# Kernel tuning notes

Measured on AMD Instinct MI355X. Metric: run time of the kernel, lower is better.

Reference implementation:

```python
import jax, jax.numpy as jnp
import numpy as np

N = 100000
E = 1600000
IN_DIM, H1, H2, H3 = 128, 128, 64, 32


def gcn_conv(x, edge_index, W, b, n):
    # PyG GCNConv (default): add self-loops, symmetric norm D^-1/2 (A+I) D^-1/2,
    # out[dst] = sum_{src->dst} norm * (x @ W)[src] + b
    src, dst = edge_index[0], edge_index[1]
    loops = jnp.arange(n)
    src = jnp.concatenate([src, loops])
    dst = jnp.concatenate([dst, loops])
    deg = jax.ops.segment_sum(jnp.ones((src.shape[0],), dtype=x.dtype), dst, num_segments=n)
    dinv = jnp.where(deg > 0, jax.lax.rsqrt(deg), jnp.zeros((), dtype=x.dtype))
    norm = dinv[src] * dinv[dst]  # [E+N]
    h = x @ W                      # [N, out_dim] dense transform first (out_dim <= in_dim)
    msg = h[src] * norm[:, None]   # [E+N, out_dim] gather + scale
    out = jax.ops.segment_sum(msg, dst, num_segments=n)
    return out + b


def setup_inputs() -> dict:
    key = jax.random.key(0)
    ks = jax.random.split(key, 10)
    def glorot(k, shape):
        lim = np.sqrt(6.0 / (shape[0] + shape[1]))
        return jax.random.uniform(k, shape, jnp.float32, -lim, lim)
    return {
        "x": jax.random.normal(ks[0], (N, IN_DIM), jnp.float32),
        "edge_index": jax.random.randint(ks[1], (2, E), 0, N, jnp.int64),
        "W1": glorot(ks[2], (IN_DIM, H1)), "b1": jnp.zeros((H1,), jnp.float32),
        "W2": glorot(ks[3], (H1, H2)),     "b2": jnp.zeros((H2,), jnp.float32),
        "W3": glorot(ks[4], (H2, H3)),     "b3": jnp.zeros((H3,), jnp.float32),
        "Wl": glorot(ks[5], (H3, 1)),      "bl": jnp.zeros((1,), jnp.float32),
    }


def reference(x, edge_index, W1, b1, W2, b2, W3, b3, Wl, bl):
    n = x.shape[0]
    h = jax.nn.relu(gcn_conv(x, edge_index, W1, b1, n))   # dropout p=0.5 is identity in eval
    h = jax.nn.relu(gcn_conv(h, edge_index, W2, b2, n))
    h = jax.nn.relu(gcn_conv(h, edge_index, W3, b3, n))
    return jax.nn.sigmoid(h @ Wl + bl)                    # [N, 1]
```

## Files before the change

### kernel.cpp

```cpp
#include <hip/hip_runtime.h>
#include <hip/hip_fp16.h>
#include <math.h>


#define BSHIFT 8
#define BNODES (1 << BSHIFT)
#define SRCBITS 17
#define MAXB 512
#define CHUNK 16384

union H8 { float4 f4; __half2 h2[4]; };

typedef _Float16 half8 __attribute__((ext_vector_type(8)));
typedef float floatx4 __attribute__((ext_vector_type(4)));

__global__ __launch_bounds__(256) void k_hist2(const int* __restrict__ dst, int E,
                                               int* __restrict__ cnt_mat, int B) {
    __shared__ int h[MAXB];
    int tid = threadIdx.x, c = blockIdx.x;
    h[tid] = 0; h[tid + 256] = 0;
    __syncthreads();
    int base = c * CHUNK, end = min(base + CHUNK, E);
    for (int i = base + tid; i < end; i += 256)
        atomicAdd(&h[dst[i] >> BSHIFT], 1);
    __syncthreads();
    for (int b = tid; b < B; b += 256) cnt_mat[c * B + b] = h[b];
}

__global__ __launch_bounds__(256) void k_colscan(const int* __restrict__ cnt_mat,
                                                 int* __restrict__ rel_mat,
                                                 int* __restrict__ total,
                                                 int B, int nchunks) {
    __shared__ int s[256];
    int b = blockIdx.x, tid = threadIdx.x;
    int v = (tid < nchunks) ? cnt_mat[tid * B + b] : 0;
    s[tid] = v;
    __syncthreads();
    for (int off = 1; off < 256; off <<= 1) {
        int t = (tid >= off) ? s[tid - off] : 0;
        __syncthreads();
        s[tid] += t;
        __syncthreads();
    }
    if (tid < nchunks) rel_mat[tid * B + b] = s[tid] - v;
    if (tid == 255) total[b] = s[255];
}

__global__ __launch_bounds__(512) void k_bscan(const int* __restrict__ total,
                                               int* __restrict__ bucketbase,
                                               int* __restrict__ row_ptr,
                                               int B, int n, int E) {
    __shared__ int s[MAXB];
    int tid = threadIdx.x;
    int v = (tid < B) ? total[tid] : 0;
    s[tid] = v;
    __syncthreads();
    for (int off = 1; off < MAXB; off <<= 1) {
        int t = (tid >= off) ? s[tid - off] : 0;
        __syncthreads();
        s[tid] += t;
        __syncthreads();
    }
    if (tid < B) bucketbase[tid] = s[tid] - v;
    if (tid == 0) { bucketbase[B] = E; row_ptr[n] = E; }
}

__global__ __launch_bounds__(256) void k_bucket2(const int* __restrict__ src,
                                                 const int* __restrict__ dst, int E,
                                                 const int* __restrict__ bucketbase,
                                                 const int* __restrict__ rel_mat,
                                                 unsigned int* __restrict__ edgebuf,
                                                 int B) {
    __shared__ int cur[MAXB];
    int c = blockIdx.x, tid = threadIdx.x;
    int base = c * CHUNK, end = min(base + CHUNK, E);
    for (int b = tid; b < B; b += 256) cur[b] = bucketbase[b] + rel_mat[c * B + b];
    __syncthreads();
    for (int i = base + tid; i < end; i += 256) {
        int d = dst[i];
        int b = d >> BSHIFT;
        unsigned int pk = ((unsigned int)(d & (BNODES - 1)) << SRCBITS) | (unsigned int)src[i];
        int pos = atomicAdd(&cur[b], 1);
        edgebuf[pos] = pk;
    }
}

__global__ __launch_bounds__(256) void k_build(const unsigned int* __restrict__ edgebuf,
                                               const int* __restrict__ bucketbase,
                                               int* __restrict__ row_ptr,
                                               float* __restrict__ dinv,
                                               int* __restrict__ col, int n) {
    __shared__ int cnt[BNODES];
    __shared__ int s[BNODES];
    int b = blockIdx.x;
    int tid = threadIdx.x;
    int node0 = b << BSHIFT;
    int ebase = bucketbase[b], eend = bucketbase[b + 1];
    cnt[tid] = 0;
    __syncthreads();
    for (int i = ebase + tid; i < eend; i += 256)
        atomicAdd(&cnt[edgebuf[i] >> SRCBITS], 1);
    __syncthreads();
    int c = cnt[tid];
    s[tid] = c;
    __syncthreads();
    for (int off = 1; off < 256; off <<= 1) {
        int t = (tid >= off) ? s[tid - off] : 0;
        __syncthreads();
        s[tid] += t;
        __syncthreads();
    }
    int p = ebase + s[tid] - c;
    int node = node0 + tid;
    if (node < n) { row_ptr[node] = p; dinv[node] = rsqrtf((float)(c + 1)); }
    cnt[tid] = p;
    __syncthreads();
    for (int i = ebase + tid; i < eend; i += 256) {
        unsigned int pk = edgebuf[i];
        int pos = atomicAdd(&cnt[pk >> SRCBITS], 1);
        col[pos] = (int)(pk & ((1u << SRCBITS) - 1));
    }
}

__global__ void k_packW3(const float* __restrict__ W1, const float* __restrict__ W2,
                         const float* __restrict__ W3, _Float16* __restrict__ P1,
                         _Float16* __restrict__ P2, _Float16* __restrict__ P3) {
    int e = blockIdx.x * 256 + threadIdx.x;
    const float* W; _Float16* P; int OUT, idx;
    if (e < 16384)      { W = W1; P = P1; OUT = 128; idx = e; }
    else if (e < 24576) { W = W2; P = P2; OUT = 64;  idx = e - 16384; }
    else if (e < 26624) { W = W3; P = P3; OUT = 32;  idx = e - 24576; }
    else return;
    int j = idx & 7;
    int lane = (idx >> 3) & 63;
    int rest = idx >> 9;
    int NT = OUT >> 4;
    int t = rest % NT;
    int ss = rest / NT;
    int k = ss * 32 + (lane >> 4) * 8 + j;
    int nn = t * 16 + (lane & 15);
    P[idx] = (_Float16)W[k * OUT + nn];
}

template <int IN, int OUT>
__global__ __launch_bounds__(256) void k_matmul_mfma(const float* __restrict__ x,
                                                     const _Float16* __restrict__ Wpk,
                                                     const float* __restrict__ dinv,
                                                     __half* __restrict__ out, int n) {
    constexpr int S = IN / 32;
    constexpr int NT = OUT / 16;
    constexpr int LDH = IN + 8;
    __shared__ _Float16 xs[64 * LDH];

    int tid = threadIdx.x;
    int rowbase = blockIdx.x * 64;

    constexpr int TOT = 64 * IN / 8;
    const float4* x4 = (const float4*)x;
    for (int i = tid; i < TOT; i += 256) {
        int r = i / (IN / 8), kg = i % (IN / 8);
        int row = rowbase + r;
        float4 a = make_float4(0.f, 0.f, 0.f, 0.f), b = a;
        if (row < n) {
            a = x4[(size_t)row * (IN / 4) + kg * 2 + 0];
            b = x4[(size_t)row * (IN / 4) + kg * 2 + 1];
        }
        H8 u;
        u.h2[0] = __float22half2_rn(make_float2(a.x, a.y));
        u.h2[1] = __float22half2_rn(make_float2(a.z, a.w));
        u.h2[2] = __float22half2_rn(make_float2(b.x, b.y));
        u.h2[3] = __float22half2_rn(make_float2(b.z, b.w));
        *(float4*)&xs[r * LDH + kg * 8] = u.f4;
    }
    __syncthreads();

    int lane = tid & 63;
    int wave = tid >> 6;
    int m = lane & 15, quad = lane >> 4;

    floatx4 acc[NT];
#pragma unroll
    for (int t = 0; t < NT; ++t) acc[t] = (floatx4){0.f, 0.f, 0.f, 0.f};

    const half8* Wf = (const half8*)Wpk;
#pragma unroll
    for (int s = 0; s < S; ++s) {
        half8 a = *(const half8*)&xs[(wave * 16 + m) * LDH + s * 32 + quad * 8];
#pragma unroll
        for (int t = 0; t < NT; ++t) {
            half8 b = Wf[(s * NT + t) * 64 + lane];
            acc[t] = __builtin_amdgcn_mfma_f32_16x16x32_f16(a, b, acc[t], 0, 0, 0);
        }
    }

    int rbase = rowbase + wave * 16 + quad * 4;
#pragma unroll
    for (int r = 0; r < 4; ++r) {
        int row = rbase + r;
        if (row < n) {
            float dsc = dinv[row];
#pragma unroll
            for (int t = 0; t < NT; ++t)
                out[(size_t)row * OUT + t * 16 + m] = __float2half(acc[t][r] * dsc);
        }
    }
}

template <int F, int OUT>
__global__ __launch_bounds__(256) void k_agg_mm(const __half* __restrict__ hs,
                                                const float* __restrict__ dinv,
                                                const float* __restrict__ bias,
                                                const int* __restrict__ row_ptr,
                                                const int* __restrict__ col,
                                                const _Float16* __restrict__ Wpk,
                                                __half* __restrict__ out, int n) {
    constexpr int S = F / 32;
    constexpr int NT = OUT / 16;
    constexpr int LDH = F + 8;
    constexpr int LPN = F / 8;
    __shared__ _Float16 zs[64 * LDH];

    int tid = threadIdx.x;
    int rowbase = blockIdx.x * 64;
    const float4* h4 = (const float4*)hs;

    for (int task = tid; task < 64 * LPN; task += 256) {
        int nl = task / LPN;
        int fg = task % LPN;
        int node = rowbase + nl;
        H8 o;
        if (node < n) {
            float acc[8];
            H8 u;
            u.f4 = h4[(size_t)node * LPN + fg];
#pragma unroll
            for (int q = 0; q < 4; ++q) {
                float2 f = __half22float2(u.h2[q]);
                acc[2 * q + 0] = f.x;
                acc[2 * q + 1] = f.y;
            }
            int beg = row_ptr[node], end = row_ptr[node + 1];
            int j = beg;
            for (; j + 3 < end; j += 4) {
                int s0 = col[j], s1 = col[j + 1], s2 = col[j + 2], s3 = col[j + 3];
                H8 u0, u1, u2, u3;
                u0.f4 = h4[(size_t)s0 * LPN + fg];
                u1.f4 = h4[(size_t)s1 * LPN + fg];
                u2.f4 = h4[(size_t)s2 * LPN + fg];
                u3.f4 = h4[(size_t)s3 * LPN + fg];
#pragma unroll
                for (int q = 0; q < 4; ++q) {
                    float2 f0 = __half22float2(u0.h2[q]);
                    float2 f1 = __half22float2(u1.h2[q]);
                    float2 f2 = __half22float2(u2.h2[q]);
                    float2 f3 = __half22float2(u3.h2[q]);
                    acc[2 * q + 0] += (f0.x + f1.x) + (f2.x + f3.x);
                    acc[2 * q + 1] += (f0.y + f1.y) + (f2.y + f3.y);
                }
            }
            for (; j < end; ++j) {
                H8 u2;
                u2.f4 = h4[(size_t)col[j] * LPN + fg];
#pragma unroll
                for (int q = 0; q < 4; ++q) {
                    float2 f = __half22float2(u2.h2[q]);
                    acc[2 * q + 0] += f.x;
                    acc[2 * q + 1] += f.y;
                }
            }
            float dsc = dinv[node];
#pragma unroll
            for (int q = 0; q < 4; ++q) {
                float v0 = fmaxf(fmaf(acc[2 * q + 0], dsc, bias[fg * 8 + 2 * q + 0]), 0.f);
                float v1 = fmaxf(fmaf(acc[2 * q + 1], dsc, bias[fg * 8 + 2 * q + 1]), 0.f);
                o.h2[q] = __floats2half2_rn(v0, v1);
            }
        } else {
            o.f4 = make_float4(0.f, 0.f, 0.f, 0.f);
        }
        *(float4*)&zs[nl * LDH + fg * 8] = o.f4;
    }
    __syncthreads();

    int lane = tid & 63;
    int wave = tid >> 6;
    int m = lane & 15, quad = lane >> 4;

    floatx4 acc[NT];
#pragma unroll
    for (int t = 0; t < NT; ++t) acc[t] = (floatx4){0.f, 0.f, 0.f, 0.f};

    const half8* Wf = (const half8*)Wpk;
#pragma unroll
    for (int s = 0; s < S; ++s) {
        half8 a = *(const half8*)&zs[(wave * 16 + m) * LDH + s * 32 + quad * 8];
#pragma unroll
        for (int t = 0; t < NT; ++t) {
            half8 b = Wf[(s * NT + t) * 64 + lane];
            acc[t] = __builtin_amdgcn_mfma_f32_16x16x32_f16(a, b, acc[t], 0, 0, 0);
        }
    }

    int rbase = rowbase + wave * 16 + quad * 4;
#pragma unroll
    for (int r = 0; r < 4; ++r) {
        int row = rbase + r;
        if (row < n) {
            float dsc = dinv[row];
#pragma unroll
            for (int t = 0; t < NT; ++t)
                out[(size_t)row * OUT + t * 16 + m] = __float2half(acc[t][r] * dsc);
        }
    }
}

__global__ __launch_bounds__(256) void k_agg_final(const __half* __restrict__ hs,
                                                   const float* __restrict__ dinv,
                                                   const float* __restrict__ bias,
                                                   const int* __restrict__ row_ptr,
                                                   const int* __restrict__ col,
                                                   const float* __restrict__ Wl,
                                                   const float* __restrict__ bl,
                                                   float* __restrict__ out, int n) {
    constexpr int LPN = 4;
    int t = blockIdx.x * 256 + threadIdx.x;
    int node = t / LPN;
    int fg = t % LPN;
    if (node >= n) return;

    const float4* h4 = (const float4*)hs;
    float acc[8];
    {
        H8 u;
        u.f4 = h4[(size_t)node * LPN + fg];
#pragma unroll
        for (int q = 0; q < 4; ++q) {
            float2 f = __half22float2(u.h2[q]);
            acc[2 * q + 0] = f.x;
            acc[2 * q + 1] = f.y;
        }
    }
    int beg = row_ptr[node], end = row_ptr[node + 1];
    int j = beg;
    for (; j + 3 < end; j += 4) {
        int s0 = col[j], s1 = col[j + 1], s2 = col[j + 2], s3 = col[j + 3];
        H8 u0, u1, u2, u3;
        u0.f4 = h4[(size_t)s0 * LPN + fg];
        u1.f4 = h4[(size_t)s1 * LPN + fg];
        u2.f4 = h4[(size_t)s2 * LPN + fg];
        u3.f4 = h4[(size_t)s3 * LPN + fg];
#pragma unroll
        for (int q = 0; q < 4; ++q) {
            float2 f0 = __half22float2(u0.h2[q]);
            float2 f1 = __half22float2(u1.h2[q]);
            float2 f2 = __half22float2(u2.h2[q]);
            float2 f3 = __half22float2(u3.h2[q]);
            acc[2 * q + 0] += (f0.x + f1.x) + (f2.x + f3.x);
            acc[2 * q + 1] += (f0.y + f1.y) + (f2.y + f3.y);
        }
    }
    for (; j < end; ++j) {
        H8 u;
        u.f4 = h4[(size_t)col[j] * LPN + fg];
#pragma unroll
        for (int q = 0; q < 4; ++q) {
            float2 f = __half22float2(u.h2[q]);
            acc[2 * q + 0] += f.x;
            acc[2 * q + 1] += f.y;
        }
    }
    float dsc = dinv[node];
    float partial = 0.f;
#pragma unroll
    for (int k = 0; k < 8; ++k) {
        float v = fmaxf(fmaf(acc[k], dsc, bias[fg * 8 + k]), 0.f);
        partial = fmaf(v, Wl[fg * 8 + k], partial);
    }
    partial += __shfl_xor(partial, 1);
    partial += __shfl_xor(partial, 2);
    if (fg == 0) out[node] = 1.f / (1.f + expf(-(partial + bl[0])));
}

extern "C" void kernel_launch(void* const* d_in, const int* in_sizes, int n_in,
                              void* d_out, int out_size, void* d_ws, size_t ws_size,
                              hipStream_t stream) {
    const float* x  = (const float*)d_in[0];
    const int*   ei = (const int*)d_in[1];
    const float* W1 = (const float*)d_in[2];
    const float* b1 = (const float*)d_in[3];
    const float* W2 = (const float*)d_in[4];
    const float* b2 = (const float*)d_in[5];
    const float* W3 = (const float*)d_in[6];
    const float* b3 = (const float*)d_in[7];
    const float* Wl = (const float*)d_in[8];
    const float* bl = (const float*)d_in[9];

    const int N = in_sizes[0] / 128;
    const int E = in_sizes[1] / 2;
    const int* src = ei;
    const int* dst = ei + E;
    const int B = (N + BNODES - 1) >> BSHIFT;
    const int NC = (E + CHUNK - 1) / CHUNK;

    char* ws = (char*)d_ws;
    size_t off = 0;
    auto take = [&](size_t bytes) -> char* {
        char* p = ws + off;
        off += (bytes + 255) & ~(size_t)255;
        return p;
    };
    int*          cnt_mat    = (int*)take((size_t)NC * B * 4);
    int*          rel_mat    = (int*)take((size_t)NC * B * 4);
    int*          total      = (int*)take(MAXB * 4);
    int*          bucketbase = (int*)take((MAXB + 1) * 4);
    unsigned int* edgebuf    = (unsigned int*)take((size_t)E * 4);
    int*          row_ptr    = (int*)take((size_t)(N + 1) * 4);
    float*        dinv       = (float*)take((size_t)N * 4);
    int*          col        = (int*)take((size_t)E * 4);
    __half*       bufA       = (__half*)take((size_t)N * 128 * 2);
    __half*       bufB       = (__half*)take((size_t)N * 128 * 2);
    _Float16*     Wpk1       = (_Float16*)take(128 * 128 * 2);
    _Float16*     Wpk2       = (_Float16*)take(128 * 64 * 2);
    _Float16*     Wpk3       = (_Float16*)take(64 * 32 * 2);
    (void)ws_size;

    int gM = (N + 63) / 64;

    k_hist2<<<NC, 256, 0, stream>>>(dst, E, cnt_mat, B);
    k_colscan<<<B, 256, 0, stream>>>(cnt_mat, rel_mat, total, B, NC);
    k_bscan<<<1, MAXB, 0, stream>>>(total, bucketbase, row_ptr, B, N, E);
    k_bucket2<<<NC, 256, 0, stream>>>(src, dst, E, bucketbase, rel_mat, edgebuf, B);
    k_build<<<B, 256, 0, stream>>>(edgebuf, bucketbase, row_ptr, dinv, col, N);

    k_packW3<<<(26624 + 255) / 256, 256, 0, stream>>>(W1, W2, W3, Wpk1, Wpk2, Wpk3);

    k_matmul_mfma<128, 128><<<gM, 256, 0, stream>>>(x, Wpk1, dinv, bufA, N);

    k_agg_mm<128, 64><<<gM, 256, 0, stream>>>(bufA, dinv, b1, row_ptr, col, Wpk2, bufB, N);

    k_agg_mm<64, 32><<<gM, 256, 0, stream>>>(bufB, dinv, b2, row_ptr, col, Wpk3, bufA, N);

    k_agg_final<<<((size_t)N * 4 + 255) / 256, 256, 0, stream>>>(
        bufA, dinv, b3, row_ptr, col, Wl, bl, (float*)d_out, N);
}
```

Baseline: 297.9 us.

## Split fused aggregate-matmul into feature-sliced gather and separate MFMA matmul

Replaces the fused aggregate+matmul kernels with separate steps. The matmul writes its output in 16-feature slices, one contiguous slice array per feature group. A new aggregation kernel then gathers one slice at a time across node blocks, so each gathered working set is a narrow 32-byte row per node, which is meant to improve cache hit rates on random neighbor gathers. The cost is extra kernel launches and an extra full write and read of the aggregated features between the gather and the matmul.

```diff
diff --git a/kernel.cpp b/kernel.cpp
--- a/kernel.cpp
+++ b/kernel.cpp
@@ -142,11 +142,12 @@
     P[idx] = (_Float16)W[k * OUT + nn];
 }
 
-template <int IN, int OUT>
-__global__ __launch_bounds__(256) void k_matmul_mfma(const float* __restrict__ x,
+template <int IN, int OUT, bool XHALF, bool SLICED>
+__global__ __launch_bounds__(256) void k_matmul_mfma(const void* __restrict__ xv,
                                                      const _Float16* __restrict__ Wpk,
                                                      const float* __restrict__ dinv,
-                                                     __half* __restrict__ out, int n) {
+                                                     __half* __restrict__ out, int n,
+                                                     int n16) {
     constexpr int S = IN / 32;
     constexpr int NT = OUT / 16;
     constexpr int LDH = IN + 8;
@@ -156,21 +157,27 @@
     int rowbase = blockIdx.x * 64;
 
     constexpr int TOT = 64 * IN / 8;
-    const float4* x4 = (const float4*)x;
+    const float4* x4 = (const float4*)xv;
     for (int i = tid; i < TOT; i += 256) {
         int r = i / (IN / 8), kg = i % (IN / 8);
         int row = rowbase + r;
-        float4 a = make_float4(0.f, 0.f, 0.f, 0.f), b = a;
-        if (row < n) {
-            a = x4[(size_t)row * (IN / 4) + kg * 2 + 0];
-            b = x4[(size_t)row * (IN / 4) + kg * 2 + 1];
-        }
-        H8 u;
-        u.h2[0] = __float22half2_rn(make_float2(a.x, a.y));
-        u.h2[1] = __float22half2_rn(make_float2(a.z, a.w));
-        u.h2[2] = __float22half2_rn(make_float2(b.x, b.y));
-        u.h2[3] = __float22half2_rn(make_float2(b.z, b.w));
-        *(float4*)&xs[r * LDH + kg * 8] = u.f4;
+        if (XHALF) {
+            float4 v = make_float4(0.f, 0.f, 0.f, 0.f);
+            if (row < n) v = x4[(size_t)row * (IN / 8) + kg];
+            *(float4*)&xs[r * LDH + kg * 8] = v;
+        } else {
+            float4 a = make_float4(0.f, 0.f, 0.f, 0.f), b = a;
+            if (row < n) {
+                a = x4[(size_t)row * (IN / 4) + kg * 2 + 0];
+                b = x4[(size_t)row * (IN / 4) + kg * 2 + 1];
+            }
+            H8 u;
+            u.h2[0] = __float22half2_rn(make_float2(a.x, a.y));
+            u.h2[1] = __float22half2_rn(make_float2(a.z, a.w));
+            u.h2[2] = __float22half2_rn(make_float2(b.x, b.y));
+            u.h2[3] = __float22half2_rn(make_float2(b.z, b.w));
+            *(float4*)&xs[r * LDH + kg * 8] = u.f4;
+        }
     }
     __syncthreads();
 
@@ -200,118 +207,81 @@
         if (row < n) {
             float dsc = dinv[row];
 #pragma unroll
-            for (int t = 0; t < NT; ++t)
-                out[(size_t)row * OUT + t * 16 + m] = __float2half(acc[t][r] * dsc);
-        }
-    }
-}
-
-template <int F, int OUT>
-__global__ __launch_bounds__(256) void k_agg_mm(const __half* __restrict__ hs,
-                                                const float* __restrict__ dinv,
-                                                const float* __restrict__ bias,
-                                                const int* __restrict__ row_ptr,
-                                                const int* __restrict__ col,
-                                                const _Float16* __restrict__ Wpk,
-                                                __half* __restrict__ out, int n) {
-    constexpr int S = F / 32;
-    constexpr int NT = OUT / 16;
-    constexpr int LDH = F + 8;
-    constexpr int LPN = F / 8;
-    __shared__ _Float16 zs[64 * LDH];
-
+            for (int t = 0; t < NT; ++t) {
+                __half v = __float2half(acc[t][r] * dsc);
+                if (SLICED) out[((size_t)t * n16 + row) * 16 + m] = v;
+                else        out[(size_t)row * OUT + t * 16 + m] = v;
+            }
+        }
+    }
+}
+
+template <int F, int NSL>
+__global__ __launch_bounds__(256) void k_agg_slice(const __half* __restrict__ hs_s,
+                                                   const float* __restrict__ dinv,
+                                                   const float* __restrict__ bias,
+                                                   const int* __restrict__ row_ptr,
+                                                   const int* __restrict__ col,
+                                                   __half* __restrict__ z, int n,
+                                                   int n16) {
+    int fg = blockIdx.x % NSL;
+    int nr = blockIdx.x / NSL;
     int tid = threadIdx.x;
-    int rowbase = blockIdx.x * 64;
-    const float4* h4 = (const float4*)hs;
-
-    for (int task = tid; task < 64 * LPN; task += 256) {
-        int nl = task / LPN;
-        int fg = task % LPN;
-        int node = rowbase + nl;
-        H8 o;
-        if (node < n) {
-            float acc[8];
-            H8 u;
-            u.f4 = h4[(size_t)node * LPN + fg];
-#pragma unroll
-            for (int q = 0; q < 4; ++q) {
-                float2 f = __half22float2(u.h2[q]);
-                acc[2 * q + 0] = f.x;
-                acc[2 * q + 1] = f.y;
-            }
-            int beg = row_ptr[node], end = row_ptr[node + 1];
-            int j = beg;
-            for (; j + 3 < end; j += 4) {
-                int s0 = col[j], s1 = col[j + 1], s2 = col[j + 2], s3 = col[j + 3];
-                H8 u0, u1, u2, u3;
-                u0.f4 = h4[(size_t)s0 * LPN + fg];
-                u1.f4 = h4[(size_t)s1 * LPN + fg];
-                u2.f4 = h4[(size_t)s2 * LPN + fg];
-                u3.f4 = h4[(size_t)s3 * LPN + fg];
-#pragma unroll
-                for (int q = 0; q < 4; ++q) {
-                    float2 f0 = __half22float2(u0.h2[q]);
-                    float2 f1 = __half22float2(u1.h2[q]);
-                    float2 f2 = __half22float2(u2.h2[q]);
-                    float2 f3 = __half22float2(u3.h2[q]);
-                    acc[2 * q + 0] += (f0.x + f1.x) + (f2.x + f3.x);
-                    acc[2 * q + 1] += (f0.y + f1.y) + (f2.y + f3.y);
-                }
-            }
-            for (; j < end; ++j) {
-                H8 u2;
-                u2.f4 = h4[(size_t)col[j] * LPN + fg];
-#pragma unroll
-                for (int q = 0; q < 4; ++q) {
-                    float2 f = __half22float2(u2.h2[q]);
-                    acc[2 * q + 0] += f.x;
-                    acc[2 * q + 1] += f.y;
-                }
-            }
-            float dsc = dinv[node];
-#pragma unroll
-            for (int q = 0; q < 4; ++q) {
-                float v0 = fmaxf(fmaf(acc[2 * q + 0], dsc, bias[fg * 8 + 2 * q + 0]), 0.f);
-                float v1 = fmaxf(fmaf(acc[2 * q + 1], dsc, bias[fg * 8 + 2 * q + 1]), 0.f);
-                o.h2[q] = __floats2half2_rn(v0, v1);
-            }
-        } else {
-            o.f4 = make_float4(0.f, 0.f, 0.f, 0.f);
-        }
-        *(float4*)&zs[nl * LDH + fg * 8] = o.f4;
-    }
-    __syncthreads();
-
-    int lane = tid & 63;
-    int wave = tid >> 6;
-    int m = lane & 15, quad = lane >> 4;
-
-    floatx4 acc[NT];
-#pragma unroll
-    for (int t = 0; t < NT; ++t) acc[t] = (floatx4){0.f, 0.f, 0.f, 0.f};
-
-    const half8* Wf = (const half8*)Wpk;
-#pragma unroll
-    for (int s = 0; s < S; ++s) {
-        half8 a = *(const half8*)&zs[(wave * 16 + m) * LDH + s * 32 + quad * 8];
-#pragma unroll
-        for (int t = 0; t < NT; ++t) {
-            half8 b = Wf[(s * NT + t) * 64 + lane];
-            acc[t] = __builtin_amdgcn_mfma_f32_16x16x32_f16(a, b, acc[t], 0, 0, 0);
-        }
-    }
-
-    int rbase = rowbase + wave * 16 + quad * 4;
-#pragma unroll
-    for (int r = 0; r < 4; ++r) {
-        int row = rbase + r;
-        if (row < n) {
-            float dsc = dinv[row];
-#pragma unroll
-            for (int t = 0; t < NT; ++t)
-                out[(size_t)row * OUT + t * 16 + m] = __float2half(acc[t][r] * dsc);
-        }
-    }
+    int node = nr * 128 + (tid >> 1);
+    int sub = tid & 1;
+    if (node >= n) return;
+
+    const float4* h4 = (const float4*)(hs_s + (size_t)fg * n16 * 16);
+    float acc[8];
+    {
+        H8 u;
+        u.f4 = h4[(size_t)node * 2 + sub];
+#pragma unroll
+        for (int q = 0; q < 4; ++q) {
+            float2 f = __half22float2(u.h2[q]);
+            acc[2 * q + 0] = f.x;
+            acc[2 * q + 1] = f.y;
+        }
+    }
+    int beg = row_ptr[node], end = row_ptr[node + 1];
+    int j = beg;
+    for (; j + 3 < end; j += 4) {
+        int s0 = col[j], s1 = col[j + 1], s2 = col[j + 2], s3 = col[j + 3];
+        H8 u0, u1, u2, u3;
+        u0.f4 = h4[(size_t)s0 * 2 + sub];
+        u1.f4 = h4[(size_t)s1 * 2 + sub];
+        u2.f4 = h4[(size_t)s2 * 2 + sub];
+        u3.f4 = h4[(size_t)s3 * 2 + sub];
+#pragma unroll
+        for (int q = 0; q < 4; ++q) {
+            float2 f0 = __half22float2(u0.h2[q]);
+            float2 f1 = __half22float2(u1.h2[q]);
+            float2 f2 = __half22float2(u2.h2[q]);
+            float2 f3 = __half22float2(u3.h2[q]);
+            acc[2 * q + 0] += (f0.x + f1.x) + (f2.x + f3.x);
+            acc[2 * q + 1] += (f0.y + f1.y) + (f2.y + f3.y);
+        }
+    }
+    for (; j < end; ++j) {
+        H8 u;
+        u.f4 = h4[(size_t)col[j] * 2 + sub];
+#pragma unroll
+        for (int q = 0; q < 4; ++q) {
+            float2 f = __half22float2(u.h2[q]);
+            acc[2 * q + 0] += f.x;
+            acc[2 * q + 1] += f.y;
+        }
+    }
+    float dsc = dinv[node];
+    int fbase = fg * 16 + sub * 8;
+    H8 o;
+#pragma unroll
+    for (int q = 0; q < 4; ++q) {
+        float v0 = fmaxf(fmaf(acc[2 * q + 0], dsc, bias[fbase + 2 * q + 0]), 0.f);
+        float v1 = fmaxf(fmaf(acc[2 * q + 1], dsc, bias[fbase + 2 * q + 1]), 0.f);
+        o.h2[q] = __floats2half2_rn(v0, v1);
+    }
+    *(float4*)(z + (size_t)node * F + fbase) = o.f4;
 }
 
 __global__ __launch_bounds__(256) void k_agg_final(const __half* __restrict__ hs,
@@ -401,6 +371,7 @@
     const int* dst = ei + E;
     const int B = (N + BNODES - 1) >> BSHIFT;
     const int NC = (E + CHUNK - 1) / CHUNK;
+    const int N16 = (N + 127) & ~127;
 
     char* ws = (char*)d_ws;
     size_t off = 0;
@@ -417,8 +388,8 @@
     int*          row_ptr    = (int*)take((size_t)(N + 1) * 4);
     float*        dinv       = (float*)take((size_t)N * 4);
     int*          col        = (int*)take((size_t)E * 4);
-    __half*       bufA       = (__half*)take((size_t)N * 128 * 2);
-    __half*       bufB       = (__half*)take((size_t)N * 128 * 2);
+    __half*       bufA       = (__half*)take((size_t)N16 * 128 * 2);
+    __half*       bufB       = (__half*)take((size_t)N16 * 128 * 2);
     _Float16*     Wpk1       = (_Float16*)take(128 * 128 * 2);
     _Float16*     Wpk2       = (_Float16*)take(128 * 64 * 2);
     _Float16*     Wpk3       = (_Float16*)take(64 * 32 * 2);
@@ -434,12 +405,15 @@
 
     k_packW3<<<(26624 + 255) / 256, 256, 0, stream>>>(W1, W2, W3, Wpk1, Wpk2, Wpk3);
 
-    k_matmul_mfma<128, 128><<<gM, 256, 0, stream>>>(x, Wpk1, dinv, bufA, N);
-
-    k_agg_mm<128, 64><<<gM, 256, 0, stream>>>(bufA, dinv, b1, row_ptr, col, Wpk2, bufB, N);
-
-    k_agg_mm<64, 32><<<gM, 256, 0, stream>>>(bufB, dinv, b2, row_ptr, col, Wpk3, bufA, N);
-
+    k_matmul_mfma<128, 128, false, true><<<gM, 256, 0, stream>>>(x, Wpk1, dinv, bufA, N, N16);
+    k_agg_slice<128, 8><<<((N + 127) / 128) * 8, 256, 0, stream>>>(
+        bufA, dinv, b1, row_ptr, col, bufB, N, N16);
+
+    k_matmul_mfma<128, 64, true, true><<<gM, 256, 0, stream>>>(bufB, Wpk2, dinv, bufA, N, N16);
+    k_agg_slice<64, 4><<<((N + 127) / 128) * 4, 256, 0, stream>>>(
+        bufA, dinv, b2, row_ptr, col, bufB, N, N16);
+
+    k_matmul_mfma<64, 32, true, false><<<gM, 256, 0, stream>>>(bufB, Wpk3, dinv, bufA, N, N16);
     k_agg_final<<<((size_t)N * 4 + 255) / 256, 256, 0, stream>>>(
         bufA, dinv, b3, row_ptr, col, Wl, bl, (float*)d_out, N);
 }
```

Measured after the change: 376.1 us. 1.26x slower.

## Fuse CSR preprocessing scans into partition and first matmul into CSR build

Applied to the files above, without the earlier changes.

Merges weight packing into the histogram launch. Replaces the column and bucket scans with per-block redundant prefix computation inside the partition kernel. Fuses the first dense transform into the per-bucket CSR build kernel, reusing locally computed degree normalisation. Halves the chunk size. This removes several kernel launches and intermediate buffers, at the cost of redundant scan work per block and fewer, heavier blocks for the first matmul.

```diff
diff --git a/kernel.cpp b/kernel.cpp
--- a/kernel.cpp
+++ b/kernel.cpp
@@ -7,17 +7,44 @@
 #define BNODES (1 << BSHIFT)
 #define SRCBITS 17
 #define MAXB 512
-#define CHUNK 16384
+#define CHUNK 8192
+#define PACKB 104
 
 union H8 { float4 f4; __half2 h2[4]; };
 
 typedef _Float16 half8 __attribute__((ext_vector_type(8)));
 typedef float floatx4 __attribute__((ext_vector_type(4)));
 
-__global__ __launch_bounds__(256) void k_hist2(const int* __restrict__ dst, int E,
-                                               int* __restrict__ cnt_mat, int B) {
+__global__ __launch_bounds__(256) void k_hist_pack(const int* __restrict__ dst, int E,
+                                                   int* __restrict__ cnt_mat, int B,
+                                                   int NC,
+                                                   const float* __restrict__ W1,
+                                                   const float* __restrict__ W2,
+                                                   const float* __restrict__ W3,
+                                                   _Float16* __restrict__ P1,
+                                                   _Float16* __restrict__ P2,
+                                                   _Float16* __restrict__ P3) {
+    int tid = threadIdx.x;
+    if ((int)blockIdx.x >= NC) {
+        int e = ((int)blockIdx.x - NC) * 256 + tid;
+        const float* W; _Float16* P; int OUT, idx;
+        if (e < 16384)      { W = W1; P = P1; OUT = 128; idx = e; }
+        else if (e < 24576) { W = W2; P = P2; OUT = 64;  idx = e - 16384; }
+        else if (e < 26624) { W = W3; P = P3; OUT = 32;  idx = e - 24576; }
+        else return;
+        int j = idx & 7;
+        int lane = (idx >> 3) & 63;
+        int rest = idx >> 9;
+        int NT = OUT >> 4;
+        int t = rest % NT;
+        int ss = rest / NT;
+        int k = ss * 32 + (lane >> 4) * 8 + j;
+        int nn = t * 16 + (lane & 15);
+        P[idx] = (_Float16)W[k * OUT + nn];
+        return;
+    }
     __shared__ int h[MAXB];
-    int tid = threadIdx.x, c = blockIdx.x;
+    int c = blockIdx.x;
     h[tid] = 0; h[tid + 256] = 0;
     __syncthreads();
     int base = c * CHUNK, end = min(base + CHUNK, E);
@@ -27,14 +54,34 @@
     for (int b = tid; b < B; b += 256) cnt_mat[c * B + b] = h[b];
 }
 
-__global__ __launch_bounds__(256) void k_colscan(const int* __restrict__ cnt_mat,
-                                                 int* __restrict__ rel_mat,
-                                                 int* __restrict__ total,
-                                                 int B, int nchunks) {
+__global__ __launch_bounds__(256) void k_part(const int* __restrict__ src,
+                                              const int* __restrict__ dst, int E,
+                                              const int* __restrict__ cnt_mat,
+                                              unsigned int* __restrict__ edgebuf,
+                                              int* __restrict__ bucketbase_g,
+                                              int* __restrict__ row_ptr,
+                                              int B, int NC, int n) {
+    __shared__ int tot[MAXB];
+    __shared__ int cur[MAXB];
     __shared__ int s[256];
-    int b = blockIdx.x, tid = threadIdx.x;
-    int v = (tid < nchunks) ? cnt_mat[tid * B + b] : 0;
-    s[tid] = v;
+    int c = blockIdx.x, tid = threadIdx.x;
+    tot[tid] = 0; tot[tid + 256] = 0;
+    cur[tid] = 0; cur[tid + 256] = 0;
+    __syncthreads();
+    for (int b = tid; b < B; b += 256) {
+        int t = 0, cp = 0;
+        for (int cc = 0; cc < NC; ++cc) {
+            int v = cnt_mat[cc * B + b];
+            t += v;
+            if (cc < c) cp += v;
+        }
+        tot[b] = t;
+        cur[b] = cp;
+    }
+    __syncthreads();
+    int a0 = tot[2 * tid], a1 = tot[2 * tid + 1];
+    int pair = a0 + a1;
+    s[tid] = pair;
     __syncthreads();
     for (int off = 1; off < 256; off <<= 1) {
         int t = (tid >= off) ? s[tid - off] : 0;
@@ -42,40 +89,17 @@
         s[tid] += t;
         __syncthreads();
     }
-    if (tid < nchunks) rel_mat[tid * B + b] = s[tid] - v;
-    if (tid == 255) total[b] = s[255];
-}
-
-__global__ __launch_bounds__(512) void k_bscan(const int* __restrict__ total,
-                                               int* __restrict__ bucketbase,
-                                               int* __restrict__ row_ptr,
-                                               int B, int n, int E) {
-    __shared__ int s[MAXB];
-    int tid = threadIdx.x;
-    int v = (tid < B) ? total[tid] : 0;
-    s[tid] = v;
-    __syncthreads();
-    for (int off = 1; off < MAXB; off <<= 1) {
-        int t = (tid >= off) ? s[tid - off] : 0;
-        __syncthreads();
-        s[tid] += t;
-        __syncthreads();
-    }
-    if (tid < B) bucketbase[tid] = s[tid] - v;
-    if (tid == 0) { bucketbase[B] = E; row_ptr[n] = E; }
-}
-
-__global__ __launch_bounds__(256) void k_bucket2(const int* __restrict__ src,
-                                                 const int* __restrict__ dst, int E,
-                                                 const int* __restrict__ bucketbase,
-                                                 const int* __restrict__ rel_mat,
-                                                 unsigned int* __restrict__ edgebuf,
-                                                 int B) {
-    __shared__ int cur[MAXB];
-    int c = blockIdx.x, tid = threadIdx.x;
+    int e0 = s[tid] - pair;
+    int e1 = e0 + a0;
+    cur[2 * tid] += e0;
+    cur[2 * tid + 1] += e1;
+    if (c == 0) {
+        if (2 * tid < B) bucketbase_g[2 * tid] = e0;
+        if (2 * tid + 1 < B) bucketbase_g[2 * tid + 1] = e1;
+        if (tid == 0) { bucketbase_g[B] = E; row_ptr[n] = E; }
+    }
+    __syncthreads();
     int base = c * CHUNK, end = min(base + CHUNK, E);
-    for (int b = tid; b < B; b += 256) cur[b] = bucketbase[b] + rel_mat[c * B + b];
-    __syncthreads();
     for (int i = base + tid; i < end; i += 256) {
         int d = dst[i];
         int b = d >> BSHIFT;
@@ -85,34 +109,47 @@
     }
 }
 
-__global__ __launch_bounds__(256) void k_build(const unsigned int* __restrict__ edgebuf,
-                                               const int* __restrict__ bucketbase,
-                                               int* __restrict__ row_ptr,
-                                               float* __restrict__ dinv,
-                                               int* __restrict__ col, int n) {
+__global__ __launch_bounds__(256) void k_buildmm(const unsigned int* __restrict__ edgebuf,
+                                                 const int* __restrict__ bucketbase,
+                                                 int* __restrict__ row_ptr,
+                                                 float* __restrict__ dinv_g,
+                                                 int* __restrict__ col,
+                                                 const float* __restrict__ x,
+                                                 const _Float16* __restrict__ Wpk1,
+                                                 __half* __restrict__ out, int n) {
+    constexpr int IN = 128, OUT = 128;
+    constexpr int S = IN / 32;
+    constexpr int NT = OUT / 16;
+    constexpr int LDH = IN + 8;
     __shared__ int cnt[BNODES];
-    __shared__ int s[BNODES];
+    __shared__ int sc[BNODES];
+    __shared__ float dloc[BNODES];
+    __shared__ _Float16 xs[64 * LDH];
+
     int b = blockIdx.x;
     int tid = threadIdx.x;
     int node0 = b << BSHIFT;
     int ebase = bucketbase[b], eend = bucketbase[b + 1];
+
     cnt[tid] = 0;
     __syncthreads();
     for (int i = ebase + tid; i < eend; i += 256)
         atomicAdd(&cnt[edgebuf[i] >> SRCBITS], 1);
     __syncthreads();
     int c = cnt[tid];
-    s[tid] = c;
+    sc[tid] = c;
     __syncthreads();
     for (int off = 1; off < 256; off <<= 1) {
-        int t = (tid >= off) ? s[tid - off] : 0;
-        __syncthreads();
-        s[tid] += t;
-        __syncthreads();
-    }
-    int p = ebase + s[tid] - c;
+        int t = (tid >= off) ? sc[tid - off] : 0;
+        __syncthreads();
+        sc[tid] += t;
+        __syncthreads();
+    }
+    int p = ebase + sc[tid] - c;
     int node = node0 + tid;
-    if (node < n) { row_ptr[node] = p; dinv[node] = rsqrtf((float)(c + 1)); }
+    float dv = rsqrtf((float)(c + 1));
+    if (node < n) { row_ptr[node] = p; dinv_g[node] = dv; }
+    dloc[tid] = dv;
     cnt[tid] = p;
     __syncthreads();
     for (int i = ebase + tid; i < eend; i += 256) {
@@ -120,88 +157,56 @@
         int pos = atomicAdd(&cnt[pk >> SRCBITS], 1);
         col[pos] = (int)(pk & ((1u << SRCBITS) - 1));
     }
-}
-
-__global__ void k_packW3(const float* __restrict__ W1, const float* __restrict__ W2,
-                         const float* __restrict__ W3, _Float16* __restrict__ P1,
-                         _Float16* __restrict__ P2, _Float16* __restrict__ P3) {
-    int e = blockIdx.x * 256 + threadIdx.x;
-    const float* W; _Float16* P; int OUT, idx;
-    if (e < 16384)      { W = W1; P = P1; OUT = 128; idx = e; }
-    else if (e < 24576) { W = W2; P = P2; OUT = 64;  idx = e - 16384; }
-    else if (e < 26624) { W = W3; P = P3; OUT = 32;  idx = e - 24576; }
-    else return;
-    int j = idx & 7;
-    int lane = (idx >> 3) & 63;
-    int rest = idx >> 9;
-    int NT = OUT >> 4;
-    int t = rest % NT;
-    int ss = rest / NT;
-    int k = ss * 32 + (lane >> 4) * 8 + j;
-    int nn = t * 16 + (lane & 15);
-    P[idx] = (_Float16)W[k * OUT + nn];
-}
-
-template <int IN, int OUT>
-__global__ __launch_bounds__(256) void k_matmul_mfma(const float* __restrict__ x,
-                                                     const _Float16* __restrict__ Wpk,
-                                                     const float* __restrict__ dinv,
-                                                     __half* __restrict__ out, int n) {
-    constexpr int S = IN / 32;
-    constexpr int NT = OUT / 16;
-    constexpr int LDH = IN + 8;
-    __shared__ _Float16 xs[64 * LDH];
-
-    int tid = threadIdx.x;
-    int rowbase = blockIdx.x * 64;
-
-    constexpr int TOT = 64 * IN / 8;
-    const float4* x4 = (const float4*)x;
-    for (int i = tid; i < TOT; i += 256) {
-        int r = i / (IN / 8), kg = i % (IN / 8);
-        int row = rowbase + r;
-        float4 a = make_float4(0.f, 0.f, 0.f, 0.f), b = a;
-        if (row < n) {
-            a = x4[(size_t)row * (IN / 4) + kg * 2 + 0];
-            b = x4[(size_t)row * (IN / 4) + kg * 2 + 1];
-        }
-        H8 u;
-        u.h2[0] = __float22half2_rn(make_float2(a.x, a.y));
-        u.h2[1] = __float22half2_rn(make_float2(a.z, a.w));
-        u.h2[2] = __float22half2_rn(make_float2(b.x, b.y));
-        u.h2[3] = __float22half2_rn(make_float2(b.z, b.w));
-        *(float4*)&xs[r * LDH + kg * 8] = u.f4;
-    }
-    __syncthreads();
 
     int lane = tid & 63;
     int wave = tid >> 6;
     int m = lane & 15, quad = lane >> 4;
-
-    floatx4 acc[NT];
-#pragma unroll
-    for (int t = 0; t < NT; ++t) acc[t] = (floatx4){0.f, 0.f, 0.f, 0.f};
-
-    const half8* Wf = (const half8*)Wpk;
-#pragma unroll
-    for (int s = 0; s < S; ++s) {
-        half8 a = *(const half8*)&xs[(wave * 16 + m) * LDH + s * 32 + quad * 8];
-#pragma unroll
-        for (int t = 0; t < NT; ++t) {
-            half8 b = Wf[(s * NT + t) * 64 + lane];
-            acc[t] = __builtin_amdgcn_mfma_f32_16x16x32_f16(a, b, acc[t], 0, 0, 0);
-        }
-    }
-
-    int rbase = rowbase + wave * 16 + quad * 4;
-#pragma unroll
-    for (int r = 0; r < 4; ++r) {
-        int row = rbase + r;
-        if (row < n) {
-            float dsc = dinv[row];
-#pragma unroll
-            for (int t = 0; t < NT; ++t)
-                out[(size_t)row * OUT + t * 16 + m] = __float2half(acc[t][r] * dsc);
+    const float4* x4 = (const float4*)x;
+    const half8* Wf = (const half8*)Wpk1;
+
+    for (int t4 = 0; t4 < 4; ++t4) {
+        int rowbase = node0 + t4 * 64;
+        __syncthreads();
+        constexpr int TOT = 64 * IN / 8;
+        for (int i = tid; i < TOT; i += 256) {
+            int r = i / (IN / 8), kg = i % (IN / 8);
+            int row = rowbase + r;
+            float4 a = make_float4(0.f, 0.f, 0.f, 0.f), bb = a;
+            if (row < n) {
+                a = x4[(size_t)row * (IN / 4) + kg * 2 + 0];
+                bb = x4[(size_t)row * (IN / 4) + kg * 2 + 1];
+            }
+            H8 u;
+            u.h2[0] = __float22half2_rn(make_float2(a.x, a.y));
+            u.h2[1] = __float22half2_rn(make_float2(a.z, a.w));
+            u.h2[2] = __float22half2_rn(make_float2(bb.x, bb.y));
+            u.h2[3] = __float22half2_rn(make_float2(bb.z, bb.w));
+            *(float4*)&xs[r * LDH + kg * 8] = u.f4;
+        }
+        __syncthreads();
+
+        floatx4 acc[NT];
+#pragma unroll
+        for (int t = 0; t < NT; ++t) acc[t] = (floatx4){0.f, 0.f, 0.f, 0.f};
+#pragma unroll
+        for (int ss = 0; ss < S; ++ss) {
+            half8 a = *(const half8*)&xs[(wave * 16 + m) * LDH + ss * 32 + quad * 8];
+#pragma unroll
+            for (int t = 0; t < NT; ++t) {
+                half8 bb = Wf[(ss * NT + t) * 64 + lane];
+                acc[t] = __builtin_amdgcn_mfma_f32_16x16x32_f16(a, bb, acc[t], 0, 0, 0);
+            }
+        }
+        int rloc = t4 * 64 + wave * 16 + quad * 4;
+#pragma unroll
+        for (int r = 0; r < 4; ++r) {
+            int row = node0 + rloc + r;
+            if (row < n) {
+                float dsc = dloc[rloc + r];
+#pragma unroll
+                for (int t = 0; t < NT; ++t)
+                    out[(size_t)row * OUT + t * 16 + m] = __float2half(acc[t][r] * dsc);
+            }
         }
     }
 }
@@ -410,8 +415,6 @@
         return p;
     };
     int*          cnt_mat    = (int*)take((size_t)NC * B * 4);
-    int*          rel_mat    = (int*)take((size_t)NC * B * 4);
-    int*          total      = (int*)take(MAXB * 4);
     int*          bucketbase = (int*)take((MAXB + 1) * 4);
     unsigned int* edgebuf    = (unsigned int*)take((size_t)E * 4);
     int*          row_ptr    = (int*)take((size_t)(N + 1) * 4);
@@ -426,20 +429,14 @@
 
     int gM = (N + 63) / 64;
 
-    k_hist2<<<NC, 256, 0, stream>>>(dst, E, cnt_mat, B);
-    k_colscan<<<B, 256, 0, stream>>>(cnt_mat, rel_mat, total, B, NC);
-    k_bscan<<<1, MAXB, 0, stream>>>(total, bucketbase, row_ptr, B, N, E);
-    k_bucket2<<<NC, 256, 0, stream>>>(src, dst, E, bucketbase, rel_mat, edgebuf, B);
-    k_build<<<B, 256, 0, stream>>>(edgebuf, bucketbase, row_ptr, dinv, col, N);
-
-    k_packW3<<<(26624 + 255) / 256, 256, 0, stream>>>(W1, W2, W3, Wpk1, Wpk2, Wpk3);
-
-    k_matmul_mfma<128, 128><<<gM, 256, 0, stream>>>(x, Wpk1, dinv, bufA, N);
-
+    k_hist_pack<<<NC + PACKB, 256, 0, stream>>>(dst, E, cnt_mat, B, NC,
+                                                W1, W2, W3, Wpk1, Wpk2, Wpk3);
+    k_part<<<NC, 256, 0, stream>>>(src, dst, E, cnt_mat, edgebuf, bucketbase,
+                                   row_ptr, B, NC, N);
+    k_buildmm<<<B, 256, 0, stream>>>(edgebuf, bucketbase, row_ptr, dinv, col,
+                                     x, Wpk1, bufA, N);
     k_agg_mm<128, 64><<<gM, 256, 0, stream>>>(bufA, dinv, b1, row_ptr, col, Wpk2, bufB, N);
-
     k_agg_mm<64, 32><<<gM, 256, 0, stream>>>(bufB, dinv, b2, row_ptr, col, Wpk3, bufA, N);
-
     k_agg_final<<<((size_t)N * 4 + 255) / 256, 256, 0, stream>>>(
         bufA, dinv, b3, row_ptr, col, Wl, bl, (float*)d_out, N);
 }
```

Result: slower. 372.7 us (+25.1%).
